# Optimization experiments

Measured on AMD Instinct MI355X. Metric: run time of the kernel, lower is better.

Reference implementation:

```python
import jax, jax.numpy as jnp
import numpy as np

NX, NF = 8192, 8192
F_SIZE, OUT_SIZE, D_ATT = 512, 256, 128
N_GRAPHS = 16
NEG_INF = -1e9


def setup_inputs() -> dict:
    key = jax.random.key(0)
    ks = jax.random.split(key, 10)
    f = jax.random.normal(ks[0], (NF, F_SIZE), dtype=jnp.float32)
    x = jax.random.normal(ks[1], (NX, OUT_SIZE), dtype=jnp.float32)
    h = jax.random.normal(ks[2], (NX, OUT_SIZE), dtype=jnp.float32)
    edge_index = jax.random.randint(ks[3], (2, NX), 0, NX)
    edge_type = jax.random.randint(ks[4], (NX,), 0, 4)
    f_batch = jnp.sort(jax.random.randint(ks[5], (NF,), 0, N_GRAPHS))
    x_batch = jnp.sort(jax.random.randint(ks[6], (NX,), 0, N_GRAPHS))
    x_init = jax.random.normal(ks[7], (NX, OUT_SIZE), dtype=jnp.float32)
    # Glorot-initialized projection weights, stored [in, out]
    def glorot(k, shape):
        lim = np.sqrt(6.0 / (shape[0] + shape[1]))
        return jax.random.uniform(k, shape, jnp.float32, -lim, lim)
    W_h = glorot(ks[8], (OUT_SIZE, D_ATT))
    kk, kv = jax.random.split(ks[9])
    W_key = glorot(kk, (F_SIZE, D_ATT))
    W_value = glorot(kv, (F_SIZE, OUT_SIZE))
    return {"f": f, "x": x, "h": h, "edge_index": edge_index,
            "edge_type": edge_type, "f_batch": f_batch, "x_batch": x_batch,
            "x_init": x_init, "W_h": W_h, "W_key": W_key, "W_value": W_value}


def reference(f, x, h, edge_index, edge_type, f_batch, x_batch, x_init,
              W_h, W_key, W_value):
    # QKV projections (bias-free linears)
    query = h @ W_h          # [Nx, 128]
    key = f @ W_key          # [Nf, 128]
    value = f @ W_value      # [Nf, out_size]
    # Block-diagonal batch mask: attend only within the same graph
    not_same = x_batch[:, None] != f_batch[None, :]       # [Nx, Nf]
    scores = jnp.einsum('qd,kd->qk', query, key)          # [Nx, Nf]
    scores = jnp.where(not_same, NEG_INF, scores)
    attn = jax.nn.softmax(scores, axis=-1)
    context = attn @ value                                 # [Nx, out_size]
    return context, attn
```

## Files before the change

kernel.cpp:

```cpp
#include <hip/hip_runtime.h>

#define NX_  8192
#define NF_  8192
#define DQ_  128
#define OUT_ 256
#define FS_  512

typedef float  f32x4  __attribute__((ext_vector_type(4)));
typedef short  bf16x8 __attribute__((ext_vector_type(8)));

static __device__ __forceinline__ void nt_store4(const float4& w, float* p) {
  f32x4 v; v.x = w.x; v.y = w.y; v.z = w.z; v.w = w.w;
  __builtin_nontemporal_store(v, (f32x4*)p);
}
static __device__ __forceinline__ ushort f2bf(float f) {
  union { float f; uint u; } c; c.f = f;
  uint r = c.u + 0x7FFF + ((c.u >> 16) & 1);
  return (ushort)(r >> 16);
}
static __device__ __forceinline__ float bf2f(ushort u) {
  union { uint u; float f; } c; c.u = ((uint)u) << 16; return c.f;
}

__global__ void ranges_kernel(const int* __restrict__ xb, const int* __restrict__ fb,
                              int* __restrict__ rng) {
  int t = threadIdx.x;
  if (t < 17) {
    int lo = 0, hi = NX_;
    while (lo < hi) { int mid = (lo + hi) >> 1; if (xb[mid] < t) lo = mid + 1; else hi = mid; }
    rng[t] = lo;
  } else if (t < 34) {
    int g = t - 17;
    int lo = 0, hi = NF_;
    while (lo < hi) { int mid = (lo + hi) >> 1; if (fb[mid] < g) lo = mid + 1; else hi = mid; }
    rng[17 + g] = lo;
  }
}

__global__ __launch_bounds__(256) void wprep_kernel(const float* __restrict__ Wh,
                                                    const float* __restrict__ Wk,
                                                    const float* __restrict__ Wv,
                                                    ushort* __restrict__ WhTh, ushort* __restrict__ WhTl,
                                                    ushort* __restrict__ WkTh, ushort* __restrict__ WkTl,
                                                    ushort* __restrict__ WvTh, ushort* __restrict__ WvTl) {
  int idx = blockIdx.x * 256 + threadIdx.x;
  float w; ushort* ph; ushort* pl; int off;
  if (idx < 32768) {
    int n = idx >> 8, k = idx & 255;
    w = Wh[k * DQ_ + n]; ph = WhTh; pl = WhTl; off = idx;
  } else if (idx < 98304) {
    int i = idx - 32768; int n = i >> 9, k = i & 511;
    w = Wk[k * DQ_ + n]; ph = WkTh; pl = WkTl; off = i;
  } else if (idx < 229376) {
    int i = idx - 98304; int n = i >> 9, k = i & 511;
    w = Wv[k * OUT_ + n]; ph = WvTh; pl = WvTl; off = i;
  } else return;
  ushort hi = f2bf(w);
  ph[off] = hi;
  pl[off] = f2bf(w - bf2f(hi));
}

__global__ __launch_bounds__(256) void prep_split(const float* __restrict__ f,
                                                  const float* __restrict__ h,
                                                  ushort* __restrict__ fh, ushort* __restrict__ fl,
                                                  ushort* __restrict__ hh, ushort* __restrict__ hl) {
  const int NF4 = (NF_ * FS_) / 4;
  const int NH4 = (NX_ * OUT_) / 4;
  int stride = gridDim.x * 256;
  for (int i = blockIdx.x * 256 + threadIdx.x; i < NF4 + NH4; i += stride) {
    const float4* src; ushort* ph; ushort* pl; int j;
    if (i < NF4) { src = (const float4*)f; ph = fh; pl = fl; j = i; }
    else         { src = (const float4*)h; ph = hh; pl = hl; j = i - NF4; }
    float4 v = src[j];
    ushort4 uh, ul;
    uh.x = f2bf(v.x); ul.x = f2bf(v.x - bf2f(uh.x));
    uh.y = f2bf(v.y); ul.y = f2bf(v.y - bf2f(uh.y));
    uh.z = f2bf(v.z); ul.z = f2bf(v.z - bf2f(uh.z));
    uh.w = f2bf(v.w); ul.w = f2bf(v.w - bf2f(uh.w));
    ((ushort4*)ph)[j] = uh;
    ((ushort4*)pl)[j] = ul;
  }
}

__global__ __launch_bounds__(256) void gemm_all(const ushort* __restrict__ fh, const ushort* __restrict__ fl,
                                                const ushort* __restrict__ hh, const ushort* __restrict__ hl,
                                                const ushort* __restrict__ WhTh, const ushort* __restrict__ WhTl,
                                                const ushort* __restrict__ WkTh, const ushort* __restrict__ WkTl,
                                                const ushort* __restrict__ WvTh,
                                                ushort* __restrict__ Qh, ushort* __restrict__ Ql,
                                                ushort* __restrict__ Kh, ushort* __restrict__ Kl,
                                                ushort* __restrict__ VT) {
  __shared__ ushort Ahi[64][64], Alo[64][64];
  __shared__ ushort Bhi[64][64], Blo[64][64];
  int bid = blockIdx.x;
  const ushort *Ah, *Al, *BTh, *BTl;
  int N, K, lid, mode;
  if (bid < 256)      { Ah = hh; Al = hl; BTh = WhTh; BTl = WhTl; N = DQ_;  K = OUT_; mode = 0; lid = bid; }
  else if (bid < 512) { Ah = fh; Al = fl; BTh = WkTh; BTl = WkTl; N = DQ_;  K = FS_;  mode = 1; lid = bid - 256; }
  else                { Ah = fh; Al = fh; BTh = WvTh; BTl = WvTh; N = OUT_; K = FS_;  mode = 2; lid = bid - 512; }
  int nbn = N >> 6;
  int bm = (lid / nbn) << 6, bn = (lid % nbn) << 6;
  int tid = threadIdx.x, lane = tid & 63, w = tid >> 6;
  int srow = tid >> 2, skq = (tid & 3) << 4;
  bool split = (mode < 2);
  f32x4 acc[4];
#pragma unroll
  for (int i = 0; i < 4; ++i) acc[i] = (f32x4){0.f, 0.f, 0.f, 0.f};

  for (int k0 = 0; k0 < K; k0 += 64) {
    size_t aoff = (size_t)(bm + srow) * K + k0 + skq;
    size_t boff = (size_t)(bn + srow) * K + k0 + skq;
#pragma unroll
    for (int j = 0; j < 2; ++j) {
      int sk = (skq + (j << 3)) ^ ((srow & 7) << 3);
      *(uint4*)&Ahi[srow][sk] = *(const uint4*)(Ah + aoff + (j << 3));
      *(uint4*)&Bhi[srow][sk] = *(const uint4*)(BTh + boff + (j << 3));
      if (split) {
        *(uint4*)&Alo[srow][sk] = *(const uint4*)(Al + aoff + (j << 3));
        *(uint4*)&Blo[srow][sk] = *(const uint4*)(BTl + boff + (j << 3));
      }
    }
    __syncthreads();
#pragma unroll
    for (int step = 0; step < 2; ++step) {
      int kb = (step << 5) + ((lane >> 4) << 3);
      int brow = (w << 4) + (lane & 15);
      int bsk = kb ^ ((brow & 7) << 3);
      bf16x8 bh = *(const bf16x8*)&Bhi[brow][bsk];
#pragma unroll
      for (int i = 0; i < 4; ++i) {
        int ar = (i << 4) + (lane & 15);
        int ask = kb ^ ((ar & 7) << 3);
        bf16x8 ah = *(const bf16x8*)&Ahi[ar][ask];
        acc[i] = __builtin_amdgcn_mfma_f32_16x16x32_bf16(ah, bh, acc[i], 0, 0, 0);
        if (split) {
          bf16x8 bl = *(const bf16x8*)&Blo[brow][bsk];
          bf16x8 al = *(const bf16x8*)&Alo[ar][ask];
          acc[i] = __builtin_amdgcn_mfma_f32_16x16x32_bf16(al, bh, acc[i], 0, 0, 0);
          acc[i] = __builtin_amdgcn_mfma_f32_16x16x32_bf16(ah, bl, acc[i], 0, 0, 0);
        }
      }
    }
    __syncthreads();
  }
  int cr = (lane >> 4) << 2, cc = lane & 15;
  if (mode < 2) {
    ushort* Ch = (mode == 0) ? Qh : Kh;
    ushort* Cl = (mode == 0) ? Ql : Kl;
#pragma unroll
    for (int i = 0; i < 4; ++i)
#pragma unroll
      for (int r = 0; r < 4; ++r) {
        float v = acc[i][r];
        ushort hi = f2bf(v);
        size_t o = (size_t)(bm + (i << 4) + cr + r) * DQ_ + bn + (w << 4) + cc;
        Ch[o] = hi;
        Cl[o] = f2bf(v - bf2f(hi));
      }
  } else {
#pragma unroll
    for (int i = 0; i < 4; ++i) {
      ushort4 o;
      o.x = f2bf(acc[i][0]); o.y = f2bf(acc[i][1]);
      o.z = f2bf(acc[i][2]); o.w = f2bf(acc[i][3]);
      *(ushort4*)&VT[(size_t)(bn + (w << 4) + cc) * NX_ + bm + (i << 4) + cr] = o;
    }
  }
}

__global__ __launch_bounds__(512) void fused_attn(const ushort* __restrict__ Qh, const ushort* __restrict__ Ql,
                                                  const ushort* __restrict__ Kh, const ushort* __restrict__ Kl,
                                                  const ushort* __restrict__ VT,
                                                  const int* __restrict__ xb,
                                                  const int* __restrict__ rng,
                                                  float* __restrict__ attn,
                                                  float* __restrict__ ctx) {
  __shared__ ushort Pb[16][784];
  __shared__ float wred[16][16];
  int bid = blockIdx.x;
  int sb = ((bid & 7) << 6) | (bid >> 3);
  int r0 = sb << 4;
  int tid = threadIdx.x;
  int w = tid >> 6, lane = tid & 63;
  int lg = lane >> 4, li = lane & 15;
  const ushort* qrh = Qh + (size_t)(r0 + li) * DQ_ + (lg << 3);
  const ushort* qrl = Ql + (size_t)(r0 + li) * DQ_ + (lg << 3);
  bf16x8 qh[4], ql[4];
#pragma unroll
  for (int db = 0; db < 4; ++db) {
    qh[db] = *(const bf16x8*)(qrh + (db << 5));
    ql[db] = *(const bf16x8*)(qrl + (db << 5));
  }
  int g0 = xb[r0], g1 = xb[r0 + 15];
  for (int g = g0; g <= g1; ++g) {
    int rs = rng[g], re = rng[g + 1];
    int ars = (rs > r0 ? rs : r0) - r0;
    int are = (re < r0 + 16 ? re : r0 + 16) - r0;
    if (ars >= are) continue;
    int ks = rng[17 + g], ke = rng[18 + g];
    int kbase = ks & ~7;
    f32x4 s[6];
#pragma unroll
    for (int tt = 0; tt < 6; ++tt) {
      int key0 = kbase + (((tt << 3) + w) << 4);
      int krow = key0 + li; if (krow > NF_ - 1) krow = NF_ - 1;
      const ushort* krh = Kh + (size_t)krow * DQ_ + (lg << 3);
      const ushort* krl = Kl + (size_t)krow * DQ_ + (lg << 3);
      f32x4 a = (f32x4){0.f, 0.f, 0.f, 0.f};
#pragma unroll
      for (int db = 0; db < 4; ++db) {
        bf16x8 kh = *(const bf16x8*)(krh + (db << 5));
        bf16x8 kl = *(const bf16x8*)(krl + (db << 5));
        a = __builtin_amdgcn_mfma_f32_16x16x32_bf16(qh[db], kh, a, 0, 0, 0);
        a = __builtin_amdgcn_mfma_f32_16x16x32_bf16(ql[db], kh, a, 0, 0, 0);
        a = __builtin_amdgcn_mfma_f32_16x16x32_bf16(qh[db], kl, a, 0, 0, 0);
      }
      s[tt] = a;
    }
    float pm[4];
#pragma unroll
    for (int r = 0; r < 4; ++r) pm[r] = -3.0e38f;
#pragma unroll
    for (int tt = 0; tt < 6; ++tt) {
      int col = kbase + (((tt << 3) + w) << 4) + li;
      bool valid = (col >= ks) && (col < ke);
#pragma unroll
      for (int r = 0; r < 4; ++r) pm[r] = fmaxf(pm[r], valid ? s[tt][r] : -3.0e38f);
    }
#pragma unroll
    for (int r = 0; r < 4; ++r) {
      pm[r] = fmaxf(pm[r], __shfl_xor(pm[r], 1));
      pm[r] = fmaxf(pm[r], __shfl_xor(pm[r], 2));
      pm[r] = fmaxf(pm[r], __shfl_xor(pm[r], 4));
      pm[r] = fmaxf(pm[r], __shfl_xor(pm[r], 8));
    }
    if (li == 0) {
#pragma unroll
      for (int r = 0; r < 4; ++r) wred[w][(lg << 2) + r] = pm[r];
    }
    __syncthreads();
    float m[4], ps[4];
#pragma unroll
    for (int r = 0; r < 4; ++r) {
      int row = (lg << 2) + r;
      float m01 = fmaxf(wred[0][row], wred[1][row]);
      float m23 = fmaxf(wred[2][row], wred[3][row]);
      float m45 = fmaxf(wred[4][row], wred[5][row]);
      float m67 = fmaxf(wred[6][row], wred[7][row]);
      m[r] = fmaxf(fmaxf(m01, m23), fmaxf(m45, m67));
      ps[r] = 0.f;
    }
#pragma unroll
    for (int tt = 0; tt < 6; ++tt) {
      int col = kbase + (((tt << 3) + w) << 4) + li;
      bool valid = (col >= ks) && (col < ke);
#pragma unroll
      for (int r = 0; r < 4; ++r) {
        float e = valid ? __expf(s[tt][r] - m[r]) : 0.f;
        s[tt][r] = e;
        ps[r] += e;
      }
    }
#pragma unroll
    for (int r = 0; r < 4; ++r) {
      ps[r] += __shfl_xor(ps[r], 1);
      ps[r] += __shfl_xor(ps[r], 2);
      ps[r] += __shfl_xor(ps[r], 4);
      ps[r] += __shfl_xor(ps[r], 8);
    }
    if (li == 0) {
#pragma unroll
      for (int r = 0; r < 4; ++r) wred[8 + w][(lg << 2) + r] = ps[r];
    }
    __syncthreads();
    float inv[4];
#pragma unroll
    for (int r = 0; r < 4; ++r) {
      int row = (lg << 2) + r;
      float s0 = wred[8][row] + wred[9][row] + wred[10][row] + wred[11][row];
      float s1 = wred[12][row] + wred[13][row] + wred[14][row] + wred[15][row];
      inv[r] = 1.0f / (s0 + s1);
    }
#pragma unroll
    for (int tt = 0; tt < 6; ++tt) {
      int kc = (((tt << 3) + w) << 4) + li;
#pragma unroll
      for (int r = 0; r < 4; ++r)
        Pb[(lg << 2) + r][kc] = f2bf(s[tt][r] * inv[r]);
    }
    __syncthreads();
    for (int idx = tid; idx < 16 * (NF_ / 4); idx += 512) {
      int row = idx >> 11;
      if (row < ars || row >= are) continue;
      int col = (idx & 2047) << 2;
      float4 wv = make_float4(0.f, 0.f, 0.f, 0.f);
      int rel = col - kbase;
      if (rel >= 0 && rel < 768) {
        ushort4 pu = *(const ushort4*)&Pb[row][rel];
        wv.x = bf2f(pu.x); wv.y = bf2f(pu.y); wv.z = bf2f(pu.z); wv.w = bf2f(pu.w);
      }
      nt_store4(wv, attn + (size_t)(r0 + row) * NF_ + col);
    }
    int nsteps = (ke - kbase + 31) >> 5;
    f32x4 pacc[2];
#pragma unroll
    for (int ot = 0; ot < 2; ++ot) pacc[ot] = (f32x4){0.f, 0.f, 0.f, 0.f};
    for (int st = 0; st < nsteps; ++st) {
      bf16x8 pfr = *(const bf16x8*)&Pb[li][(st << 5) + (lg << 3)];
      int kaddr = kbase + (st << 5) + (lg << 3);
      if (kaddr > NF_ - 8) kaddr = NF_ - 8;
#pragma unroll
      for (int ot = 0; ot < 2; ++ot) {
        const ushort* vr = VT + (size_t)((w << 5) + (ot << 4) + li) * NX_ + kaddr;
        bf16x8 vfr = *(const bf16x8*)vr;
        pacc[ot] = __builtin_amdgcn_mfma_f32_16x16x32_bf16(pfr, vfr, pacc[ot], 0, 0, 0);
      }
    }
#pragma unroll
    for (int ot = 0; ot < 2; ++ot)
#pragma unroll
      for (int r = 0; r < 4; ++r) {
        int row = (lg << 2) + r;
        if (row >= ars && row < are)
          ctx[(size_t)(r0 + row) * OUT_ + (w << 5) + (ot << 4) + li] = pacc[ot][r];
      }
    __syncthreads();
  }
}

extern "C" void kernel_launch(void* const* d_in, const int* in_sizes, int n_in,
                              void* d_out, int out_size, void* d_ws, size_t ws_size,
                              hipStream_t stream) {
  const float* f   = (const float*)d_in[0];
  const float* h   = (const float*)d_in[2];
  const int*   fb  = (const int*)d_in[5];
  const int*   xbt = (const int*)d_in[6];
  const float* Wh  = (const float*)d_in[8];
  const float* Wk  = (const float*)d_in[9];
  const float* Wv  = (const float*)d_in[10];

  float* ctx_out  = (float*)d_out;
  float* attn_out = ctx_out + (size_t)NX_ * OUT_;

  ushort* fh   = (ushort*)d_ws;
  ushort* fl   = fh + (size_t)NF_ * FS_;
  ushort* hh   = fl + (size_t)NF_ * FS_;
  ushort* hl   = hh + (size_t)NX_ * OUT_;
  ushort* Qh   = hl + (size_t)NX_ * OUT_;
  ushort* Ql   = Qh + (size_t)NX_ * DQ_;
  ushort* Kh   = Ql + (size_t)NX_ * DQ_;
  ushort* Kl   = Kh + (size_t)NF_ * DQ_;
  ushort* VT   = Kl + (size_t)NF_ * DQ_;
  ushort* WhTh = VT + (size_t)OUT_ * NX_;
  ushort* WhTl = WhTh + 32768;
  ushort* WkTh = WhTl + 32768;
  ushort* WkTl = WkTh + 65536;
  ushort* WvTh = WkTl + 65536;
  ushort* WvTl = WvTh + 131072;
  int*    rng  = (int*)(WvTl + 131072);

  hipLaunchKernelGGL(ranges_kernel, dim3(1), dim3(64), 0, stream, xbt, fb, rng);
  hipLaunchKernelGGL(wprep_kernel, dim3(896), dim3(256), 0, stream,
                     Wh, Wk, Wv, WhTh, WhTl, WkTh, WkTl, WvTh, WvTl);
  hipLaunchKernelGGL(prep_split, dim3(2048), dim3(256), 0, stream,
                     f, h, fh, fl, hh, hl);
  hipLaunchKernelGGL(gemm_all, dim3(1024), dim3(256), 0, stream,
                     fh, fl, hh, hl, WhTh, WhTl, WkTh, WkTl, WvTh,
                     Qh, Ql, Kh, Kl, VT);
  hipLaunchKernelGGL(fused_attn, dim3(NX_ / 16), dim3(512), 0, stream,
                     Qh, Ql, Kh, Kl, VT, xbt, rng, attn_out, ctx_out);
}
```

Measured before the change: 425.7 us.

## Split dense attn writeout into separate expand kernel via compact buffer

The fused attention kernel no longer writes the full dense 8192-wide attention rows. It now stores only the in-graph probability window (up to 768 columns) in fp32 to a compact workspace buffer. A new expand_attn kernel then streams the full rows, zero-filling outside the window. The aim is to take the heavy store traffic out of the MFMA kernel and free it to run faster, at the cost of an extra launch and an extra compact write/read. The stored values also change: the new path writes fp32 probabilities, where the old path wrote bf16-rounded ones.

```diff
diff --git a/kernel.cpp b/kernel.cpp
--- a/kernel.cpp
+++ b/kernel.cpp
@@ -5,6 +5,7 @@
 #define DQ_  128
 #define OUT_ 256
 #define FS_  512
+#define PSTRIDE 800
 
 typedef float  f32x4  __attribute__((ext_vector_type(4)));
 typedef short  bf16x8 __attribute__((ext_vector_type(8)));
@@ -173,7 +174,7 @@
                                                   const ushort* __restrict__ VT,
                                                   const int* __restrict__ xb,
                                                   const int* __restrict__ rng,
-                                                  float* __restrict__ attn,
+                                                  float* __restrict__ Pc,
                                                   float* __restrict__ ctx) {
   __shared__ ushort Pb[16][784];
   __shared__ float wred[16][16];
@@ -285,22 +286,15 @@
     for (int tt = 0; tt < 6; ++tt) {
       int kc = (((tt << 3) + w) << 4) + li;
 #pragma unroll
-      for (int r = 0; r < 4; ++r)
-        Pb[(lg << 2) + r][kc] = f2bf(s[tt][r] * inv[r]);
-    }
-    __syncthreads();
-    for (int idx = tid; idx < 16 * (NF_ / 4); idx += 512) {
-      int row = idx >> 11;
-      if (row < ars || row >= are) continue;
-      int col = (idx & 2047) << 2;
-      float4 wv = make_float4(0.f, 0.f, 0.f, 0.f);
-      int rel = col - kbase;
-      if (rel >= 0 && rel < 768) {
-        ushort4 pu = *(const ushort4*)&Pb[row][rel];
-        wv.x = bf2f(pu.x); wv.y = bf2f(pu.y); wv.z = bf2f(pu.z); wv.w = bf2f(pu.w);
-      }
-      nt_store4(wv, attn + (size_t)(r0 + row) * NF_ + col);
-    }
+      for (int r = 0; r < 4; ++r) {
+        int row = (lg << 2) + r;
+        float p = s[tt][r] * inv[r];
+        Pb[row][kc] = f2bf(p);
+        if (row >= ars && row < are)
+          Pc[(size_t)(r0 + row) * PSTRIDE + kc] = p;
+      }
+    }
+    __syncthreads();
     int nsteps = (ke - kbase + 31) >> 5;
     f32x4 pacc[2];
 #pragma unroll
@@ -325,6 +319,28 @@
           ctx[(size_t)(r0 + row) * OUT_ + (w << 5) + (ot << 4) + li] = pacc[ot][r];
       }
     __syncthreads();
+  }
+}
+
+__global__ __launch_bounds__(256) void expand_attn(const float* __restrict__ Pc,
+                                                   const int* __restrict__ xb,
+                                                   const int* __restrict__ rng,
+                                                   float* __restrict__ attn) {
+  const int nhalf = NX_ * 2;
+  for (int u = blockIdx.x; u < nhalf; u += gridDim.x) {
+    int row = u >> 1, half = u & 1;
+    int kbase = rng[17 + xb[row]] & ~7;
+    const float4* pc4 = (const float4*)(Pc + (size_t)row * PSTRIDE);
+    float* arow = attn + (size_t)row * NF_ + (half << 12);
+    int c0 = (half << 12) - kbase;
+#pragma unroll
+    for (int jj = 0; jj < 4; ++jj) {
+      int j = threadIdx.x + (jj << 8);
+      int rel = c0 + (j << 2);
+      float4 wv = make_float4(0.f, 0.f, 0.f, 0.f);
+      if (rel >= 0 && rel < 768) wv = pc4[rel >> 2];
+      nt_store4(wv, arow + (j << 2));
+    }
   }
 }
 
@@ -357,7 +373,8 @@
   ushort* WkTl = WkTh + 65536;
   ushort* WvTh = WkTl + 65536;
   ushort* WvTl = WvTh + 131072;
-  int*    rng  = (int*)(WvTl + 131072);
+  float*  Pc   = (float*)(WvTl + 131072);
+  int*    rng  = (int*)(Pc + (size_t)NX_ * PSTRIDE);
 
   hipLaunchKernelGGL(ranges_kernel, dim3(1), dim3(64), 0, stream, xbt, fb, rng);
   hipLaunchKernelGGL(wprep_kernel, dim3(896), dim3(256), 0, stream,
@@ -368,5 +385,7 @@
                      fh, fl, hh, hl, WhTh, WhTl, WkTh, WkTl, WvTh,
                      Qh, Ql, Kh, Kl, VT);
   hipLaunchKernelGGL(fused_attn, dim3(NX_ / 16), dim3(512), 0, stream,
-                     Qh, Ql, Kh, Kl, VT, xbt, rng, attn_out, ctx_out);
-}
+                     Qh, Ql, Kh, Kl, VT, xbt, rng, Pc, ctx_out);
+  hipLaunchKernelGGL(expand_attn, dim3(2048), dim3(256), 0, stream,
+                     Pc, xbt, rng, attn_out);
+}
```

After: 428.8 us. Within noise of the previous version (+0.7%).
